# Kernel tuning notes

Hardware: AMD Instinct MI355X
Metric: run time of the kernel (lower is better)

Reference implementation:

```python
import jax, jax.numpy as jnp
import numpy as np

T_IN, T_OUT = 16, 25          # in_length, out_length
B, K = 4096, 32               # heroes, neighbors per hero
N = B * K                     # total neighbor tracks
ENC, DEC, DYN, EMB = 64, 128, 32, 32


def _lrelu(x):
    return jnp.where(x >= 0, x, 0.1 * x)


def _lstm(x, Wih, Whh, bih, bhh, hidden):
    """PyTorch-convention LSTM (gate order i,f,g,o). x: [T, B, D]. Returns (all_h [T,B,H], last_h [B,H])."""
    z = jnp.zeros((x.shape[1], hidden), x.dtype)

    def step(carry, xt):
        h, c = carry
        g = xt @ Wih.T + bih + h @ Whh.T + bhh
        i, f, gg, o = jnp.split(g, 4, axis=-1)
        c = jax.nn.sigmoid(f) * c + jax.nn.sigmoid(i) * jnp.tanh(gg)
        h = jax.nn.sigmoid(o) * jnp.tanh(c)
        return (h, c), h

    (h, c), hs = jax.lax.scan(step, (z, z), x)
    return hs, h


def setup_inputs() -> dict:
    key = jax.random.key(0)
    ks = jax.random.split(key, 20)
    p = lambda k, s: jax.random.normal(k, s, jnp.float32) * 0.1
    return {
        "hist": jax.random.normal(ks[0], (T_IN, B, 2), jnp.float32),
        "nbrs": jax.random.normal(ks[1], (T_IN, N, 2), jnp.float32),
        "Wip": p(ks[2], (EMB, 2)), "bip": p(ks[3], (EMB,)),
        "Wih_e": p(ks[4], (4 * ENC, EMB)), "Whh_e": p(ks[5], (4 * ENC, ENC)),
        "bih_e": p(ks[6], (4 * ENC,)), "bhh_e": p(ks[7], (4 * ENC,)),
        "Wdyn": p(ks[8], (DYN, ENC)), "bdyn": p(ks[9], (DYN,)),
        "Wnbr": p(ks[10], (ENC, 2 * T_IN)), "bnbr": p(ks[11], (ENC,)),
        "Wih_d": p(ks[12], (4 * DEC, 2 * DYN)), "Whh_d": p(ks[13], (4 * DEC, DEC)),
        "bih_d": p(ks[14], (4 * DEC,)), "bhh_d": p(ks[15], (4 * DEC,)),
        "Wop": p(ks[16], (2, DEC)), "bop": p(ks[17], (2,)),
        # index_division flattened: neighbor j belongs to hero segment_ids[j] (sorted, K per hero)
        "segment_ids": jnp.repeat(jnp.arange(B, dtype=jnp.int32), K),
    }


def reference(hist, nbrs, Wip, bip, Wih_e, Whh_e, bih_e, bhh_e, Wdyn, bdyn,
              Wnbr, bnbr, Wih_d, Whh_d, bih_d, bhh_d, Wop, bop, segment_ids):
    # --- encode ego history ---
    emb = _lrelu(hist @ Wip.T + bip)                       # [T,B,EMB]
    _, h_enc = _lstm(emb, Wih_e, Whh_e, bih_e, bhh_e, ENC)  # [B,ENC]
    hist_e = _lrelu(h_enc @ Wdyn.T + bdyn)                 # [B,DYN]

    # --- relative neighbor tracks + ragged segment-max pooling ---
    relative = hist[:, segment_ids, :] - nbrs              # [T,N,2]  (hero_repeated gather)
    rela = jnp.transpose(relative, (1, 0, 2)).reshape(N, 2 * T_IN)  # permute(1,0,2).view(-1,2*in_length)
    rela_enc = _lrelu(rela @ Wnbr.T + bnbr)                # [N,ENC]
    scene = jax.ops.segment_max(rela_enc, segment_ids, num_segments=B)  # fused per-group max
    scene = _lrelu(scene @ Wdyn.T + bdyn)                  # [B,DYN]

    # --- decode ---
    enc = jnp.concatenate([hist_e, scene], axis=1)         # [B,2*DYN]
    dec_in = jnp.broadcast_to(enc, (T_OUT, B, 2 * DYN))    # unsqueeze(0).repeat(out_length,1,1)
    h_dec, _ = _lstm(dec_in, Wih_d, Whh_d, bih_d, bhh_d, DEC)  # [T_OUT,B,DEC]
    fut = h_dec @ Wop.T + bop                              # [T_OUT,B,2]
    # outputActivation: with 2 output dims (muX,muY only) it is the identity
    return fut
```

## Files before the change

kernel.cpp:

```cpp
#include <hip/hip_runtime.h>
#include <hip/hip_bf16.h>

#define T_IN   16
#define T_OUT  25
#define BHERO  4096
#define K_NBR  32
#define N_NBR  (BHERO * K_NBR)
#define ENC    64
#define DEC    128
#define DYN    32
#define EMB    32

#define EROW   104
#define DROW   136
#define RROW   40

#define OFF_RELA   56576
#define OFF_PMAX   97536
#define OFF_ENC    113152
#define OFF_WOP    117504
#define OFF_WIP    118528
#define OFF_BIP    118784
#define OFF_BOP    118912
#define LDS_TOTAL  118928

typedef __attribute__((ext_vector_type(8))) short bf16x8;
typedef __attribute__((ext_vector_type(4))) float f32x4;

__device__ __forceinline__ float lrelu(float x) { return x >= 0.f ? x : 0.1f * x; }
__device__ __forceinline__ float rcpf(float x)  { return __builtin_amdgcn_rcpf(x); }
__device__ __forceinline__ float sigm(float x)  { return rcpf(1.f + __expf(-x)); }
__device__ __forceinline__ float tanhv(float x) {
    return fmaf(2.f, rcpf(1.f + __expf(-2.f * x)), -1.f);
}
__device__ __forceinline__ short f2bf(float x) {
    unsigned u = __float_as_uint(x);
    return (short)((u + 0x7FFFu + ((u >> 16) & 1u)) >> 16);
}
__device__ __forceinline__ float bf2f(short s) {
    return __uint_as_float(((unsigned)(unsigned short)s) << 16);
}

__global__ __launch_bounds__(512, 2) void highway_fused(
    const float* __restrict__ hist,  const float* __restrict__ nbrs,
    const float* __restrict__ Wip,   const float* __restrict__ bip,
    const float* __restrict__ WihE,  const float* __restrict__ WhhE,
    const float* __restrict__ bihE,  const float* __restrict__ bhhE,
    const float* __restrict__ Wdyn,  const float* __restrict__ bdyn,
    const float* __restrict__ Wnbr,  const float* __restrict__ bnbr,
    const float* __restrict__ WihD,  const float* __restrict__ WhhD,
    const float* __restrict__ bihD,  const float* __restrict__ bhhD,
    const float* __restrict__ Wop,   const float* __restrict__ bop,
    const int*   __restrict__ seg,
    float* __restrict__ fut)
{
    __shared__ __align__(16) char lds_raw[LDS_TOTAL];
    auto slab   = (short (*)[16][EROW])  lds_raw;
    auto rela   = (short (*)[RROW])     (lds_raw + OFF_RELA);
    auto pmax   = (float (*)[ENC])      (lds_raw + OFF_PMAX);
    auto hist_s = (short (*)[16][DROW])  lds_raw;
    auto enc_s  = (float (*)[68])       (lds_raw + OFF_ENC);
    auto wop_s  = (float (*)[DEC])      (lds_raw + OFF_WOP);
    auto wip_s  = (float (*)[2])        (lds_raw + OFF_WIP);
    auto bip_s  = (float*)              (lds_raw + OFF_BIP);
    auto bop_s  = (float*)              (lds_raw + OFF_BOP);

    const int b0  = blockIdx.x * 16;
    const int n0  = blockIdx.x * 512;
    const int tid = threadIdx.x;
    const int w = tid >> 6, l = tid & 63, r = l & 15, lg = l >> 4;

    if (tid < EMB) {
        wip_s[tid][0] = Wip[2 * tid];
        wip_s[tid][1] = Wip[2 * tid + 1];
        bip_s[tid]    = bip[tid];
    }
    if (tid < 2 * DEC) wop_s[tid >> 7][tid & 127] = Wop[tid];
    if (tid < 2)       bop_s[tid] = bop[tid];
    for (int i = tid; i < 16 * ENC; i += 512) slab[0][i >> 6][32 + (i & 63)] = 0;

    bf16x8 BfN[4];
    float  biasn[4];
    #pragma unroll
    for (int ct = 0; ct < 4; ++ct) {
        const int col = ct * 16 + r;
        biasn[ct] = bnbr[col];
        const float* src = Wnbr + (size_t)col * (2 * T_IN) + 8 * lg;
        float4 f0 = *(const float4*)src;
        float4 f1 = *(const float4*)(src + 4);
        bf16x8 bb;
        bb[0]=f2bf(f0.x); bb[1]=f2bf(f0.y); bb[2]=f2bf(f0.z); bb[3]=f2bf(f0.w);
        bb[4]=f2bf(f1.x); bb[5]=f2bf(f1.y); bb[6]=f2bf(f1.z); bb[7]=f2bf(f1.w);
        BfN[ct] = bb;
    }

    bf16x8 BfE[4][3];
    float  biasjE[4];
    if (tid < 256) {
        #pragma unroll
        for (int j = 0; j < 4; ++j) {
            const int col = j * ENC + w * 16 + r;
            biasjE[j] = bihE[col] + bhhE[col];
            #pragma unroll
            for (int c = 0; c < 3; ++c) {
                const float* src = (c == 0) ? (WihE + (size_t)col * EMB + 8 * lg)
                                            : (WhhE + (size_t)col * ENC + (c - 1) * 32 + 8 * lg);
                float4 f0 = *(const float4*)src;
                float4 f1 = *(const float4*)(src + 4);
                bf16x8 bb;
                bb[0]=f2bf(f0.x); bb[1]=f2bf(f0.y); bb[2]=f2bf(f0.z); bb[3]=f2bf(f0.w);
                bb[4]=f2bf(f1.x); bb[5]=f2bf(f1.y); bb[6]=f2bf(f1.z); bb[7]=f2bf(f1.w);
                BfE[j][c] = bb;
            }
        }
    }

    {
        const int n  = tid;
        const int hb = seg[n0 + n];
        unsigned* dst = (unsigned*)&rela[n][0];
        for (int t = 0; t < T_IN; ++t) {
            float2 hv = *(const float2*)&hist[((size_t)t * BHERO + hb) * 2];
            float2 nv = *(const float2*)&nbrs[((size_t)t * N_NBR + n0 + n) * 2];
            unsigned p = (unsigned)(unsigned short)f2bf(hv.x - nv.x)
                       | ((unsigned)(unsigned short)f2bf(hv.y - nv.y) << 16);
            dst[t] = p;
        }
    }
    __syncthreads();

    if (tid < 256) {
        const int t = tid >> 4, m = tid & 15;
        float2 hv = *(const float2*)&hist[((size_t)t * BHERO + b0 + m) * 2];
        #pragma unroll
        for (int jb = 0; jb < 4; ++jb) {
            bf16x8 v;
            #pragma unroll
            for (int e = 0; e < 8; ++e) {
                int j = jb * 8 + e;
                v[e] = f2bf(lrelu(hv.x * wip_s[j][0] + hv.y * wip_s[j][1] + bip_s[j]));
            }
            *(bf16x8*)&slab[t][m][jb * 8] = v;
        }
    }
    #pragma unroll
    for (int rr = 0; rr < 4; ++rr) {
        const int rt = w + 8 * rr;
        bf16x8 a = *(const bf16x8*)&rela[rt * 16 + r][8 * lg];
        #pragma unroll
        for (int ct = 0; ct < 4; ++ct) {
            f32x4 acc = {biasn[ct], biasn[ct], biasn[ct], biasn[ct]};
            acc = __builtin_amdgcn_mfma_f32_16x16x32_bf16(a, BfN[ct], acc, 0, 0, 0);
            float m4 = fmaxf(fmaxf(acc[0], acc[1]), fmaxf(acc[2], acc[3]));
            m4 = fmaxf(m4, __shfl_xor(m4, 16));
            m4 = fmaxf(m4, __shfl_xor(m4, 32));
            if (l < 16) pmax[rt][ct * 16 + r] = m4;
        }
    }
    f32x4 cstE = {0.f, 0.f, 0.f, 0.f};
    __syncthreads();

    for (int t = 0; t < T_IN; ++t) {
        if (tid < 256) {
            const short* rowp = &slab[t][r][0];
            bf16x8 a0 = *(const bf16x8*)(rowp + (0 + lg) * 8);
            bf16x8 a1 = *(const bf16x8*)(rowp + (4 + lg) * 8);
            bf16x8 a2 = *(const bf16x8*)(rowp + (8 + lg) * 8);
            f32x4 acc[4];
            #pragma unroll
            for (int j = 0; j < 4; ++j) {
                acc[j] = (f32x4){biasjE[j], biasjE[j], biasjE[j], biasjE[j]};
                acc[j] = __builtin_amdgcn_mfma_f32_16x16x32_bf16(a0, BfE[j][0], acc[j], 0, 0, 0);
                acc[j] = __builtin_amdgcn_mfma_f32_16x16x32_bf16(a1, BfE[j][1], acc[j], 0, 0, 0);
                acc[j] = __builtin_amdgcn_mfma_f32_16x16x32_bf16(a2, BfE[j][2], acc[j], 0, 0, 0);
            }
            #pragma unroll
            for (int q = 0; q < 4; ++q) {
                float i = sigm(acc[0][q]);
                float f = sigm(acc[1][q]);
                float g = tanhv(acc[2][q]);
                float o = sigm(acc[3][q]);
                float cc = fmaf(f, cstE[q], i * g);
                cstE[q] = cc;
                slab[t + 1][4 * lg + q][32 + w * 16 + r] = f2bf(o * tanhv(cc));
            }
        }
        __syncthreads();
    }

    #pragma unroll
    for (int it = 0; it < 2; ++it) {
        const int s = tid + 512 * it;
        const int m = s >> 6, col = s & 63;
        const float* wd = Wdyn + (size_t)(col & 31) * ENC;
        float a = bdyn[col & 31];
        if (col < 32) {
            const short* hp = &slab[T_IN][m][32];
            #pragma unroll 8
            for (int k = 0; k < ENC; ++k) a = fmaf(bf2f(hp[k]), wd[k], a);
        } else {
            #pragma unroll 8
            for (int k = 0; k < ENC; ++k) {
                float sv = lrelu(fmaxf(pmax[2 * m][k], pmax[2 * m + 1][k]));
                a = fmaf(sv, wd[k], a);
            }
        }
        enc_s[m][col] = lrelu(a);
    }
    for (int i = tid; i < 16 * DROW; i += 512) ((short*)hist_s)[i] = 0;
    __syncthreads();

    const int u0 = w * 16;
    bf16x8 BfD[4][4];
    float  biasjD[4];
    #pragma unroll
    for (int j = 0; j < 4; ++j) {
        const int col = j * DEC + u0 + r;
        biasjD[j] = bihD[col] + bhhD[col];
        #pragma unroll
        for (int c = 0; c < 4; ++c) {
            const float* src = WhhD + (size_t)col * DEC + c * 32 + 8 * lg;
            float4 f0 = *(const float4*)src;
            float4 f1 = *(const float4*)(src + 4);
            bf16x8 bb;
            bb[0]=f2bf(f0.x); bb[1]=f2bf(f0.y); bb[2]=f2bf(f0.z); bb[3]=f2bf(f0.w);
            bb[4]=f2bf(f1.x); bb[5]=f2bf(f1.y); bb[6]=f2bf(f1.z); bb[7]=f2bf(f1.w);
            BfD[j][c] = bb;
        }
    }
    f32x4 xwf[4];
    {
        bf16x8 aE[2];
        #pragma unroll
        for (int c = 0; c < 2; ++c) {
            float4 f0 = *(const float4*)&enc_s[r][c * 32 + 8 * lg];
            float4 f1 = *(const float4*)&enc_s[r][c * 32 + 8 * lg + 4];
            bf16x8 v;
            v[0]=f2bf(f0.x); v[1]=f2bf(f0.y); v[2]=f2bf(f0.z); v[3]=f2bf(f0.w);
            v[4]=f2bf(f1.x); v[5]=f2bf(f1.y); v[6]=f2bf(f1.z); v[7]=f2bf(f1.w);
            aE[c] = v;
        }
        #pragma unroll
        for (int j = 0; j < 4; ++j) {
            const int col = j * DEC + u0 + r;
            f32x4 a = {biasjD[j], biasjD[j], biasjD[j], biasjD[j]};
            #pragma unroll
            for (int c = 0; c < 2; ++c) {
                const float* src = WihD + (size_t)col * (2 * DYN) + c * 32 + 8 * lg;
                float4 f0 = *(const float4*)src;
                float4 f1 = *(const float4*)(src + 4);
                bf16x8 bb;
                bb[0]=f2bf(f0.x); bb[1]=f2bf(f0.y); bb[2]=f2bf(f0.z); bb[3]=f2bf(f0.w);
                bb[4]=f2bf(f1.x); bb[5]=f2bf(f1.y); bb[6]=f2bf(f1.z); bb[7]=f2bf(f1.w);
                a = __builtin_amdgcn_mfma_f32_16x16x32_bf16(aE[c], bb, a, 0, 0, 0);
            }
            xwf[j] = a;
        }
    }

    f32x4 cst = {0.f, 0.f, 0.f, 0.f};
    for (int t = 0; t < T_OUT; ++t) {
        const short* rowp = &hist_s[t][r][0];
        bf16x8 a_[4];
        #pragma unroll
        for (int c = 0; c < 4; ++c)
            a_[c] = *(const bf16x8*)(rowp + (4 * c + lg) * 8);
        f32x4 acc[4];
        #pragma unroll
        for (int j = 0; j < 4; ++j) {
            acc[j] = xwf[j];
            #pragma unroll
            for (int c = 0; c < 4; ++c)
                acc[j] = __builtin_amdgcn_mfma_f32_16x16x32_bf16(a_[c], BfD[j][c], acc[j], 0, 0, 0);
        }
        #pragma unroll
        for (int q = 0; q < 4; ++q) {
            float i = sigm(acc[0][q]);
            float f = sigm(acc[1][q]);
            float g = tanhv(acc[2][q]);
            float o = sigm(acc[3][q]);
            float cc = fmaf(f, cst[q], i * g);
            cst[q] = cc;
            hist_s[t + 1][4 * lg + q][u0 + r] = f2bf(o * tanhv(cc));
        }
        __syncthreads();
    }

    if (tid < T_OUT * 16) {
        const int t = tid >> 4, m = tid & 15;
        const short* hp = &hist_s[t + 1][m][0];
        float o0 = bop_s[0], o1 = bop_s[1];
        #pragma unroll
        for (int ub = 0; ub < DEC / 8; ++ub) {
            bf16x8 hv = *(const bf16x8*)(hp + ub * 8);
            #pragma unroll
            for (int e = 0; e < 8; ++e) {
                float h = bf2f(hv[e]);
                o0 = fmaf(h, wop_s[0][ub * 8 + e], o0);
                o1 = fmaf(h, wop_s[1][ub * 8 + e], o1);
            }
        }
        *(float2*)(fut + ((size_t)t * BHERO + b0 + m) * 2) = make_float2(o0, o1);
    }
}

extern "C" void kernel_launch(void* const* d_in, const int* in_sizes, int n_in,
                              void* d_out, int out_size, void* d_ws, size_t ws_size,
                              hipStream_t stream) {
    (void)d_ws; (void)ws_size; (void)in_sizes; (void)n_in; (void)out_size;
    const float* hist  = (const float*)d_in[0];
    const float* nbrs  = (const float*)d_in[1];
    const float* Wip   = (const float*)d_in[2];
    const float* bip   = (const float*)d_in[3];
    const float* Wih_e = (const float*)d_in[4];
    const float* Whh_e = (const float*)d_in[5];
    const float* bih_e = (const float*)d_in[6];
    const float* bhh_e = (const float*)d_in[7];
    const float* Wdyn  = (const float*)d_in[8];
    const float* bdyn  = (const float*)d_in[9];
    const float* Wnbr  = (const float*)d_in[10];
    const float* bnbr  = (const float*)d_in[11];
    const float* Wih_d = (const float*)d_in[12];
    const float* Whh_d = (const float*)d_in[13];
    const float* bih_d = (const float*)d_in[14];
    const float* bhh_d = (const float*)d_in[15];
    const float* Wop   = (const float*)d_in[16];
    const float* bop   = (const float*)d_in[17];
    const int*   seg   = (const int*)d_in[18];
    float* fut = (float*)d_out;

    hipLaunchKernelGGL(highway_fused, dim3(BHERO / 16), dim3(512), 0, stream,
                       hist, nbrs, Wip, bip, Wih_e, Whh_e, bih_e, bhh_e, Wdyn, bdyn,
                       Wnbr, bnbr, Wih_d, Whh_d, bih_d, bhh_d, Wop, bop, seg, fut);
}
```

Before: 64.22 us.

## Overlap neighbor encoding with encoder LSTM across warp groups and hoist decoder weights

The neighbor-track relative gather and the MFMA-plus-max pooling now run on the idle upper 256 threads, spread across the 16 encoder LSTM timesteps so they overlap the encoder recurrence instead of running before it. Decoder recurrent weights are loaded into registers at kernel start, so their global latency is hidden under the encoder work. Bf16 packing now uses the HIP paired conversion intrinsics, and the LDS read/write addresses in both recurrences are strength-reduced with loop-carried pointers. The cost is higher register pressure from holding decoder weights during the encoder phase, which may spill at a launch bound of 512 threads and 2 blocks per CU.

```diff
diff --git a/kernel.cpp b/kernel.cpp
--- a/kernel.cpp
+++ b/kernel.cpp
@@ -14,6 +14,8 @@
 #define EROW   104
 #define DROW   136
 #define RROW   40
+#define SLABE  (16 * EROW * 2)
+#define SLABD  (16 * DROW * 2)
 
 #define OFF_RELA   56576
 #define OFF_PMAX   97536
@@ -34,8 +36,16 @@
     return fmaf(2.f, rcpf(1.f + __expf(-2.f * x)), -1.f);
 }
 __device__ __forceinline__ short f2bf(float x) {
-    unsigned u = __float_as_uint(x);
-    return (short)((u + 0x7FFFu + ((u >> 16) & 1u)) >> 16);
+    __hip_bfloat16 b = __float2bfloat16(x);
+    short s; __builtin_memcpy(&s, &b, 2); return s;
+}
+__device__ __forceinline__ unsigned pk2(float lo, float hi) {
+    __hip_bfloat162 p = __float22bfloat162_rn(make_float2(lo, hi));
+    unsigned u; __builtin_memcpy(&u, &p, 4); return u;
+}
+__device__ __forceinline__ bf16x8 mk_frag(float4 f0, float4 f1) {
+    uint4 v = { pk2(f0.x, f0.y), pk2(f0.z, f0.w), pk2(f1.x, f1.y), pk2(f1.z, f1.w) };
+    bf16x8 r; __builtin_memcpy(&r, &v, 16); return r;
 }
 __device__ __forceinline__ float bf2f(short s) {
     return __uint_as_float(((unsigned)(unsigned short)s) << 16);
@@ -69,6 +79,7 @@
     const int n0  = blockIdx.x * 512;
     const int tid = threadIdx.x;
     const int w = tid >> 6, l = tid & 63, r = l & 15, lg = l >> 4;
+    const int u0 = w * 16;
 
     if (tid < EMB) {
         wip_s[tid][0] = Wip[2 * tid];
@@ -79,52 +90,44 @@
     if (tid < 2)       bop_s[tid] = bop[tid];
     for (int i = tid; i < 16 * ENC; i += 512) slab[0][i >> 6][32 + (i & 63)] = 0;
 
-    bf16x8 BfN[4];
-    float  biasn[4];
+    bf16x8 BfD[4][4];
+    float  biasjD[4];
     #pragma unroll
-    for (int ct = 0; ct < 4; ++ct) {
-        const int col = ct * 16 + r;
-        biasn[ct] = bnbr[col];
-        const float* src = Wnbr + (size_t)col * (2 * T_IN) + 8 * lg;
-        float4 f0 = *(const float4*)src;
-        float4 f1 = *(const float4*)(src + 4);
-        bf16x8 bb;
-        bb[0]=f2bf(f0.x); bb[1]=f2bf(f0.y); bb[2]=f2bf(f0.z); bb[3]=f2bf(f0.w);
-        bb[4]=f2bf(f1.x); bb[5]=f2bf(f1.y); bb[6]=f2bf(f1.z); bb[7]=f2bf(f1.w);
-        BfN[ct] = bb;
+    for (int j = 0; j < 4; ++j) {
+        const int col = j * DEC + u0 + r;
+        biasjD[j] = bihD[col] + bhhD[col];
+        #pragma unroll
+        for (int c = 0; c < 4; ++c) {
+            const float* src = WhhD + (size_t)col * DEC + c * 32 + 8 * lg;
+            BfD[j][c] = mk_frag(*(const float4*)src, *(const float4*)(src + 4));
+        }
     }
 
     bf16x8 BfE[4][3];
     float  biasjE[4];
+    bf16x8 BfN[2];
+    float  biasn[2];
     if (tid < 256) {
         #pragma unroll
         for (int j = 0; j < 4; ++j) {
-            const int col = j * ENC + w * 16 + r;
+            const int col = j * ENC + u0 + r;
             biasjE[j] = bihE[col] + bhhE[col];
             #pragma unroll
             for (int c = 0; c < 3; ++c) {
                 const float* src = (c == 0) ? (WihE + (size_t)col * EMB + 8 * lg)
                                             : (WhhE + (size_t)col * ENC + (c - 1) * 32 + 8 * lg);
-                float4 f0 = *(const float4*)src;
-                float4 f1 = *(const float4*)(src + 4);
-                bf16x8 bb;
-                bb[0]=f2bf(f0.x); bb[1]=f2bf(f0.y); bb[2]=f2bf(f0.z); bb[3]=f2bf(f0.w);
-                bb[4]=f2bf(f1.x); bb[5]=f2bf(f1.y); bb[6]=f2bf(f1.z); bb[7]=f2bf(f1.w);
-                BfE[j][c] = bb;
-            }
-        }
-    }
-
-    {
-        const int n  = tid;
-        const int hb = seg[n0 + n];
-        unsigned* dst = (unsigned*)&rela[n][0];
-        for (int t = 0; t < T_IN; ++t) {
-            float2 hv = *(const float2*)&hist[((size_t)t * BHERO + hb) * 2];
-            float2 nv = *(const float2*)&nbrs[((size_t)t * N_NBR + n0 + n) * 2];
-            unsigned p = (unsigned)(unsigned short)f2bf(hv.x - nv.x)
-                       | ((unsigned)(unsigned short)f2bf(hv.y - nv.y) << 16);
-            dst[t] = p;
+                BfE[j][c] = mk_frag(*(const float4*)src, *(const float4*)(src + 4));
+            }
+        }
+    } else {
+        const int i = w - 4;
+        const int ct0 = (i & 1) * 2;
+        #pragma unroll
+        for (int cc2 = 0; cc2 < 2; ++cc2) {
+            const int col = (ct0 + cc2) * 16 + r;
+            biasn[cc2] = bnbr[col];
+            const float* src = Wnbr + (size_t)col * (2 * T_IN) + 8 * lg;
+            BfN[cc2] = mk_frag(*(const float4*)src, *(const float4*)(src + 4));
         }
     }
     __syncthreads();
@@ -134,58 +137,95 @@
         float2 hv = *(const float2*)&hist[((size_t)t * BHERO + b0 + m) * 2];
         #pragma unroll
         for (int jb = 0; jb < 4; ++jb) {
-            bf16x8 v;
-            #pragma unroll
-            for (int e = 0; e < 8; ++e) {
-                int j = jb * 8 + e;
-                v[e] = f2bf(lrelu(hv.x * wip_s[j][0] + hv.y * wip_s[j][1] + bip_s[j]));
-            }
-            *(bf16x8*)&slab[t][m][jb * 8] = v;
-        }
-    }
-    #pragma unroll
-    for (int rr = 0; rr < 4; ++rr) {
-        const int rt = w + 8 * rr;
-        bf16x8 a = *(const bf16x8*)&rela[rt * 16 + r][8 * lg];
-        #pragma unroll
-        for (int ct = 0; ct < 4; ++ct) {
-            f32x4 acc = {biasn[ct], biasn[ct], biasn[ct], biasn[ct]};
-            acc = __builtin_amdgcn_mfma_f32_16x16x32_bf16(a, BfN[ct], acc, 0, 0, 0);
-            float m4 = fmaxf(fmaxf(acc[0], acc[1]), fmaxf(acc[2], acc[3]));
-            m4 = fmaxf(m4, __shfl_xor(m4, 16));
-            m4 = fmaxf(m4, __shfl_xor(m4, 32));
-            if (l < 16) pmax[rt][ct * 16 + r] = m4;
-        }
+            float e[8];
+            #pragma unroll
+            for (int q = 0; q < 8; ++q) {
+                int j = jb * 8 + q;
+                e[q] = lrelu(hv.x * wip_s[j][0] + hv.y * wip_s[j][1] + bip_s[j]);
+            }
+            uint4 v = { pk2(e[0],e[1]), pk2(e[2],e[3]), pk2(e[4],e[5]), pk2(e[6],e[7]) };
+            __builtin_memcpy(&slab[t][m][jb * 8], &v, 16);
+        }
+    } else {
+        const int x = tid - 256;
+        const int n  = x & 31;
+        const int ts = x >> 5;
+        const int hb = seg[n0 + n];
+        float2 h0 = *(const float2*)&hist[((size_t)ts * BHERO + hb) * 2];
+        float2 v0 = *(const float2*)&nbrs[((size_t)ts * N_NBR + n0 + n) * 2];
+        float2 h1 = *(const float2*)&hist[((size_t)(ts + 8) * BHERO + hb) * 2];
+        float2 v1 = *(const float2*)&nbrs[((size_t)(ts + 8) * N_NBR + n0 + n) * 2];
+        unsigned* dst = (unsigned*)&rela[n][0];
+        dst[ts]     = pk2(h0.x - v0.x, h0.y - v0.y);
+        dst[ts + 8] = pk2(h1.x - v1.x, h1.y - v1.y);
     }
     f32x4 cstE = {0.f, 0.f, 0.f, 0.f};
     __syncthreads();
 
-    for (int t = 0; t < T_IN; ++t) {
-        if (tid < 256) {
-            const short* rowp = &slab[t][r][0];
-            bf16x8 a0 = *(const bf16x8*)(rowp + (0 + lg) * 8);
-            bf16x8 a1 = *(const bf16x8*)(rowp + (4 + lg) * 8);
-            bf16x8 a2 = *(const bf16x8*)(rowp + (8 + lg) * 8);
-            f32x4 acc[4];
-            #pragma unroll
-            for (int j = 0; j < 4; ++j) {
-                acc[j] = (f32x4){biasjE[j], biasjE[j], biasjE[j], biasjE[j]};
-                acc[j] = __builtin_amdgcn_mfma_f32_16x16x32_bf16(a0, BfE[j][0], acc[j], 0, 0, 0);
-                acc[j] = __builtin_amdgcn_mfma_f32_16x16x32_bf16(a1, BfE[j][1], acc[j], 0, 0, 0);
-                acc[j] = __builtin_amdgcn_mfma_f32_16x16x32_bf16(a2, BfE[j][2], acc[j], 0, 0, 0);
-            }
-            #pragma unroll
-            for (int q = 0; q < 4; ++q) {
-                float i = sigm(acc[0][q]);
-                float f = sigm(acc[1][q]);
-                float g = tanhv(acc[2][q]);
-                float o = sigm(acc[3][q]);
-                float cc = fmaf(f, cstE[q], i * g);
-                cstE[q] = cc;
-                slab[t + 1][4 * lg + q][32 + w * 16 + r] = f2bf(o * tanhv(cc));
-            }
-        }
-        __syncthreads();
+    {
+        const char* rbase = lds_raw + (size_t)r * (EROW * 2);
+        char*       wbase = lds_raw + SLABE + (size_t)(4 * lg) * (EROW * 2) + (size_t)(32 + u0 + r) * 2;
+        const int   x = tid - 256;
+        #pragma unroll 1
+        for (int t = 0; t < T_IN; ++t) {
+            if (tid < 256) {
+                const short* rp = (const short*)rbase;
+                bf16x8 a0 = *(const bf16x8*)(rp + (0 + lg) * 8);
+                bf16x8 a1 = *(const bf16x8*)(rp + (4 + lg) * 8);
+                bf16x8 a2 = *(const bf16x8*)(rp + (8 + lg) * 8);
+                f32x4 acc[4];
+                #pragma unroll
+                for (int j = 0; j < 4; ++j) {
+                    acc[j] = (f32x4){biasjE[j], biasjE[j], biasjE[j], biasjE[j]};
+                    acc[j] = __builtin_amdgcn_mfma_f32_16x16x32_bf16(a0, BfE[j][0], acc[j], 0, 0, 0);
+                    acc[j] = __builtin_amdgcn_mfma_f32_16x16x32_bf16(a1, BfE[j][1], acc[j], 0, 0, 0);
+                    acc[j] = __builtin_amdgcn_mfma_f32_16x16x32_bf16(a2, BfE[j][2], acc[j], 0, 0, 0);
+                }
+                float hq[4];
+                #pragma unroll
+                for (int q = 0; q < 4; ++q) {
+                    float ii = sigm(acc[0][q]);
+                    float ff = sigm(acc[1][q]);
+                    float gg = tanhv(acc[2][q]);
+                    float oo = sigm(acc[3][q]);
+                    float cc = fmaf(ff, cstE[q], ii * gg);
+                    cstE[q] = cc;
+                    hq[q] = oo * tanhv(cc);
+                }
+                unsigned u01 = pk2(hq[0], hq[1]), u23 = pk2(hq[2], hq[3]);
+                short* wp = (short*)wbase;
+                wp[0 * EROW] = (short)u01; wp[1 * EROW] = (short)(u01 >> 16);
+                wp[2 * EROW] = (short)u23; wp[3 * EROW] = (short)(u23 >> 16);
+            } else {
+                if (t < T_IN - 1) {
+                    const int n  = 32 * (t + 1) + (x & 31);
+                    const int ts = x >> 5;
+                    const int hb = seg[n0 + n];
+                    float2 h0 = *(const float2*)&hist[((size_t)ts * BHERO + hb) * 2];
+                    float2 v0 = *(const float2*)&nbrs[((size_t)ts * N_NBR + n0 + n) * 2];
+                    float2 h1 = *(const float2*)&hist[((size_t)(ts + 8) * BHERO + hb) * 2];
+                    float2 v1 = *(const float2*)&nbrs[((size_t)(ts + 8) * N_NBR + n0 + n) * 2];
+                    unsigned* dst = (unsigned*)&rela[n][0];
+                    dst[ts]     = pk2(h0.x - v0.x, h0.y - v0.y);
+                    dst[ts + 8] = pk2(h1.x - v1.x, h1.y - v1.y);
+                }
+                const int i  = w - 4;
+                const int rt = 2 * t + (i >> 1);
+                const int ct0 = (i & 1) * 2;
+                bf16x8 a = *(const bf16x8*)&rela[rt * 16 + r][8 * lg];
+                #pragma unroll
+                for (int cc2 = 0; cc2 < 2; ++cc2) {
+                    f32x4 acc = {biasn[cc2], biasn[cc2], biasn[cc2], biasn[cc2]};
+                    acc = __builtin_amdgcn_mfma_f32_16x16x32_bf16(a, BfN[cc2], acc, 0, 0, 0);
+                    float m4 = fmaxf(fmaxf(acc[0], acc[1]), fmaxf(acc[2], acc[3]));
+                    m4 = fmaxf(m4, __shfl_xor(m4, 16));
+                    m4 = fmaxf(m4, __shfl_xor(m4, 32));
+                    if (l < 16) pmax[rt][(ct0 + cc2) * 16 + r] = m4;
+                }
+            }
+            __syncthreads();
+            rbase += SLABE; wbase += SLABE;
+        }
     }
 
     #pragma unroll
@@ -210,24 +250,6 @@
     for (int i = tid; i < 16 * DROW; i += 512) ((short*)hist_s)[i] = 0;
     __syncthreads();
 
-    const int u0 = w * 16;
-    bf16x8 BfD[4][4];
-    float  biasjD[4];
-    #pragma unroll
-    for (int j = 0; j < 4; ++j) {
-        const int col = j * DEC + u0 + r;
-        biasjD[j] = bihD[col] + bhhD[col];
-        #pragma unroll
-        for (int c = 0; c < 4; ++c) {
-            const float* src = WhhD + (size_t)col * DEC + c * 32 + 8 * lg;
-            float4 f0 = *(const float4*)src;
-            float4 f1 = *(const float4*)(src + 4);
-            bf16x8 bb;
-            bb[0]=f2bf(f0.x); bb[1]=f2bf(f0.y); bb[2]=f2bf(f0.z); bb[3]=f2bf(f0.w);
-            bb[4]=f2bf(f1.x); bb[5]=f2bf(f1.y); bb[6]=f2bf(f1.z); bb[7]=f2bf(f1.w);
-            BfD[j][c] = bb;
-        }
-    }
     f32x4 xwf[4];
     {
         bf16x8 aE[2];
@@ -235,10 +257,7 @@
         for (int c = 0; c < 2; ++c) {
             float4 f0 = *(const float4*)&enc_s[r][c * 32 + 8 * lg];
             float4 f1 = *(const float4*)&enc_s[r][c * 32 + 8 * lg + 4];
-            bf16x8 v;
-            v[0]=f2bf(f0.x); v[1]=f2bf(f0.y); v[2]=f2bf(f0.z); v[3]=f2bf(f0.w);
-            v[4]=f2bf(f1.x); v[5]=f2bf(f1.y); v[6]=f2bf(f1.z); v[7]=f2bf(f1.w);
-            aE[c] = v;
+            aE[c] = mk_frag(f0, f1);
         }
         #pragma unroll
         for (int j = 0; j < 4; ++j) {
@@ -247,43 +266,50 @@
             #pragma unroll
             for (int c = 0; c < 2; ++c) {
                 const float* src = WihD + (size_t)col * (2 * DYN) + c * 32 + 8 * lg;
-                float4 f0 = *(const float4*)src;
-                float4 f1 = *(const float4*)(src + 4);
-                bf16x8 bb;
-                bb[0]=f2bf(f0.x); bb[1]=f2bf(f0.y); bb[2]=f2bf(f0.z); bb[3]=f2bf(f0.w);
-                bb[4]=f2bf(f1.x); bb[5]=f2bf(f1.y); bb[6]=f2bf(f1.z); bb[7]=f2bf(f1.w);
-                a = __builtin_amdgcn_mfma_f32_16x16x32_bf16(aE[c], bb, a, 0, 0, 0);
+                a = __builtin_amdgcn_mfma_f32_16x16x32_bf16(
+                        aE[c], mk_frag(*(const float4*)src, *(const float4*)(src + 4)), a, 0, 0, 0);
             }
             xwf[j] = a;
         }
     }
 
     f32x4 cst = {0.f, 0.f, 0.f, 0.f};
-    for (int t = 0; t < T_OUT; ++t) {
-        const short* rowp = &hist_s[t][r][0];
-        bf16x8 a_[4];
-        #pragma unroll
-        for (int c = 0; c < 4; ++c)
-            a_[c] = *(const bf16x8*)(rowp + (4 * c + lg) * 8);
-        f32x4 acc[4];
-        #pragma unroll
-        for (int j = 0; j < 4; ++j) {
-            acc[j] = xwf[j];
+    {
+        const char* rbase = lds_raw + (size_t)r * (DROW * 2);
+        char*       wbase = lds_raw + SLABD + (size_t)(4 * lg) * (DROW * 2) + (size_t)(u0 + r) * 2;
+        #pragma unroll 1
+        for (int t = 0; t < T_OUT; ++t) {
+            const short* rp = (const short*)rbase;
+            bf16x8 a_[4];
             #pragma unroll
             for (int c = 0; c < 4; ++c)
-                acc[j] = __builtin_amdgcn_mfma_f32_16x16x32_bf16(a_[c], BfD[j][c], acc[j], 0, 0, 0);
-        }
-        #pragma unroll
-        for (int q = 0; q < 4; ++q) {
-            float i = sigm(acc[0][q]);
-            float f = sigm(acc[1][q]);
-            float g = tanhv(acc[2][q]);
-            float o = sigm(acc[3][q]);
-            float cc = fmaf(f, cst[q], i * g);
-            cst[q] = cc;
-            hist_s[t + 1][4 * lg + q][u0 + r] = f2bf(o * tanhv(cc));
-        }
-        __syncthreads();
+                a_[c] = *(const bf16x8*)(rp + (4 * c + lg) * 8);
+            f32x4 acc[4];
+            #pragma unroll
+            for (int j = 0; j < 4; ++j) {
+                acc[j] = xwf[j];
+                #pragma unroll
+                for (int c = 0; c < 4; ++c)
+                    acc[j] = __builtin_amdgcn_mfma_f32_16x16x32_bf16(a_[c], BfD[j][c], acc[j], 0, 0, 0);
+            }
+            float hq[4];
+            #pragma unroll
+            for (int q = 0; q < 4; ++q) {
+                float ii = sigm(acc[0][q]);
+                float ff = sigm(acc[1][q]);
+                float gg = tanhv(acc[2][q]);
+                float oo = sigm(acc[3][q]);
+                float cc = fmaf(ff, cst[q], ii * gg);
+                cst[q] = cc;
+                hq[q] = oo * tanhv(cc);
+            }
+            unsigned u01 = pk2(hq[0], hq[1]), u23 = pk2(hq[2], hq[3]);
+            short* wp = (short*)wbase;
+            wp[0 * DROW] = (short)u01; wp[1 * DROW] = (short)(u01 >> 16);
+            wp[2 * DROW] = (short)u23; wp[3 * DROW] = (short)(u23 >> 16);
+            __syncthreads();
+            rbase += SLABD; wbase += SLABD;
+        }
     }
 
     if (tid < T_OUT * 16) {
```

New measurement: 67.04 us. 4.4% more time.
